# Performance work log

Measured on AMD Instinct MI355X. Metric: run time of the kernel, lower is better.

The kernel has to match this reference:

```python
import jax, jax.numpy as jnp
import numpy as np

N_NODES = 100000
F_DIM = 128
D_LAT = 64
N_EDGES = 1000000
H_DIM = 128


def setup_inputs() -> dict:
    key = jax.random.key(0)
    ks = jax.random.split(key, 10)
    rng = np.random.default_rng(0)
    # positive edges (random graph) and non-edge negative pairs (dedup vs edge set,
    # mirroring the membership check in the torch elbo loop)
    edges = rng.integers(0, N_NODES, size=(2, N_EDGES))
    edge_hash = edges[0].astype(np.int64) * N_NODES + edges[1]
    cand = rng.integers(0, N_NODES, size=(2, 2 * N_EDGES))
    cand_hash = cand[0].astype(np.int64) * N_NODES + cand[1]
    keep = ~np.isin(cand_hash, edge_hash)
    neg = cand[:, keep][:, :N_EDGES]
    r = lambda k, s, sc=1.0: jax.random.normal(k, s, jnp.float32) * sc
    return {
        "x": r(ks[0], (N_NODES, F_DIM)),
        "eps": r(ks[1], (N_NODES, D_LAT)),
        "W_mu": r(ks[2], (F_DIM, D_LAT), 0.05),
        "b_mu": jnp.zeros((D_LAT,), jnp.float32),
        "W_lv": r(ks[3], (F_DIM, D_LAT), 0.05),
        "b_lv": jnp.zeros((D_LAT,), jnp.float32),
        "W1": r(ks[4], (D_LAT, H_DIM), 0.1),
        "b1": jnp.zeros((H_DIM,), jnp.float32),
        "W2": r(ks[5], (H_DIM, 1), 0.1),
        "b2": jnp.zeros((1,), jnp.float32),
        "edge_index": jnp.asarray(edges, jnp.int64) if jax.config.jax_enable_x64 else jnp.asarray(edges, jnp.int32),
        "neg_index": jnp.asarray(neg, jnp.int64) if jax.config.jax_enable_x64 else jnp.asarray(neg, jnp.int32),
    }


def reference(x, eps, W_mu, b_mu, W_lv, b_lv, W1, b1, W2, b2, edge_index, neg_index):
    # encoder: per-node diagonal Gaussian q(z|x)
    mu = x @ W_mu + b_mu            # [N, D]
    logvar = x @ W_lv + b_lv        # [N, D]
    z = mu + eps * jnp.exp(0.5 * logvar)  # q.rsample()

    def pair_logits(idx):
        zu = z[idx[0]]              # [E, D] gather
        zv = z[idx[1]]
        h = jax.nn.relu((zu * zv) @ W1 + b1)  # [E, H]
        return (h @ W2 + b2)[:, 0]  # [E]

    # Bernoulli(logits).log_prob(1) = log_sigmoid(l); log(1 - sigmoid(l)) = log_sigmoid(-l)
    true_lp = jax.nn.log_sigmoid(pair_logits(edge_index))
    false_lp = jax.nn.log_sigmoid(-pair_logits(neg_index))
    recon = jnp.mean(jnp.concatenate([true_lp, false_lp]))

    # KL(q || N(0, I)) per node, mean over nodes
    kl = jnp.mean(0.5 * jnp.sum(jnp.square(mu) + jnp.exp(logvar) - 1.0 - logvar, axis=-1))
    return -(recon - kl)
```

## Files before the change

kernel.cpp:

```cpp
#include <hip/hip_runtime.h>
#include <math.h>

#define F_DIM 128
#define D_LAT 64
#define H_DIM 128

typedef __attribute__((ext_vector_type(8))) short bf16x8;
typedef __attribute__((ext_vector_type(4))) float f32x4;
typedef __attribute__((ext_vector_type(2))) float f32x2;

__device__ __forceinline__ unsigned short f2bf(float f) {
    unsigned int u = __builtin_bit_cast(unsigned int, f);
    return (unsigned short)((u + 0x8000u) >> 16);
}

__device__ __forceinline__ long prod_fp8(unsigned long long qu, unsigned long long qv) {
    const unsigned int ul = (unsigned int)qu, uh = (unsigned int)(qu >> 32);
    const unsigned int vl = (unsigned int)qv, vh = (unsigned int)(qv >> 32);
    const f32x2 u01 = __builtin_amdgcn_cvt_pk_f32_fp8(ul, false);
    const f32x2 u23 = __builtin_amdgcn_cvt_pk_f32_fp8(ul, true);
    const f32x2 u45 = __builtin_amdgcn_cvt_pk_f32_fp8(uh, false);
    const f32x2 u67 = __builtin_amdgcn_cvt_pk_f32_fp8(uh, true);
    const f32x2 v01 = __builtin_amdgcn_cvt_pk_f32_fp8(vl, false);
    const f32x2 v23 = __builtin_amdgcn_cvt_pk_f32_fp8(vl, true);
    const f32x2 v45 = __builtin_amdgcn_cvt_pk_f32_fp8(vh, false);
    const f32x2 v67 = __builtin_amdgcn_cvt_pk_f32_fp8(vh, true);
    const f32x2 p01 = u01 * v01, p23 = u23 * v23;
    const f32x2 p45 = u45 * v45, p67 = u67 * v67;
    unsigned int r0 = __builtin_amdgcn_cvt_pk_fp8_f32(p01[0], p01[1], 0u, false);
    r0 = __builtin_amdgcn_cvt_pk_fp8_f32(p23[0], p23[1], r0, true);
    unsigned int r1 = __builtin_amdgcn_cvt_pk_fp8_f32(p45[0], p45[1], 0u, false);
    r1 = __builtin_amdgcn_cvt_pk_fp8_f32(p67[0], p67[1], r1, true);
    return (long)(((unsigned long long)r1 << 32) | r0);
}

__global__ __launch_bounds__(256) void enc_mfma_kernel(
    const float* __restrict__ x, const float* __restrict__ eps,
    const float* __restrict__ Wmu, const float* __restrict__ bmu,
    const float* __restrict__ Wlv, const float* __restrict__ blv,
    unsigned char* __restrict__ zb, float* __restrict__ accum, int nNodes)
{
    const int lane = threadIdx.x & 63;
    const int li   = lane & 15;
    const int gi   = lane >> 4;

    bf16x8 wf[8][4];
#pragma unroll
    for (int t = 0; t < 4; ++t)
#pragma unroll
        for (int s = 0; s < 4; ++s)
#pragma unroll
            for (int j = 0; j < 8; ++j) {
                const int k = s * 32 + gi * 8 + j;
                wf[t][s][j]     = (short)f2bf(Wmu[k * D_LAT + 16 * t + li]);
                wf[t + 4][s][j] = (short)f2bf(Wlv[k * D_LAT + 16 * t + li]);
            }
    float bmu4[4], blv4[4];
#pragma unroll
    for (int t = 0; t < 4; ++t) {
        bmu4[t] = bmu[16 * t + li];
        blv4[t] = blv[16 * t + li];
    }

    const int wid = (blockIdx.x * blockDim.x + threadIdx.x) >> 6;
    const int nw  = (gridDim.x * blockDim.x) >> 6;
    const int NB  = nNodes >> 4;

    float klacc = 0.f;
    for (int nb = wid; nb < NB; nb += nw) {
        const int nbase = nb << 4;
        const float* __restrict__ xrow = x + (size_t)(nbase + li) * F_DIM;

        bf16x8 af[4];
#pragma unroll
        for (int s = 0; s < 4; ++s) {
            const f32x4 v0 = *(const f32x4*)(xrow + s * 32 + gi * 8);
            const f32x4 v1 = *(const f32x4*)(xrow + s * 32 + gi * 8 + 4);
#pragma unroll
            for (int j = 0; j < 4; ++j) {
                af[s][j]     = (short)f2bf(v0[j]);
                af[s][j + 4] = (short)f2bf(v1[j]);
            }
        }

        f32x4 acc[8];
#pragma unroll
        for (int t = 0; t < 4; ++t) {
            acc[t]     = (f32x4){bmu4[t], bmu4[t], bmu4[t], bmu4[t]};
            acc[t + 4] = (f32x4){blv4[t], blv4[t], blv4[t], blv4[t]};
        }
#pragma unroll
        for (int t = 0; t < 8; ++t)
#pragma unroll
            for (int s = 0; s < 4; ++s)
                acc[t] = __builtin_amdgcn_mfma_f32_16x16x32_bf16(af[s], wf[t][s], acc[t], 0, 0, 0);

#pragma unroll
        for (int r = 0; r < 4; ++r) {
            const int row = nbase + gi * 4 + r;
#pragma unroll
            for (int t = 0; t < 4; ++t) {
                const float mu  = acc[t][r];
                const float lv  = acc[t + 4][r];
                const float e05 = __expf(0.5f * lv);
                klacc += mu * mu + e05 * e05 - 1.0f - lv;
                const float zv = fmaf(eps[(size_t)row * D_LAT + 16 * t + li], e05, mu);
                zb[(size_t)row * D_LAT + 16 * t + li] =
                    (unsigned char)(__builtin_amdgcn_cvt_pk_fp8_f32(zv, 0.f, 0u, false) & 0xffu);
            }
        }
    }
    for (int off = 32; off; off >>= 1) klacc += __shfl_xor(klacc, off);
    if (lane == 0) atomicAdd(&accum[1], 0.5f * klacc);
}

__global__ __launch_bounds__(256) void edge_mfma_kernel(
    const unsigned char* __restrict__ zb,
    const int* __restrict__ eidx, const int* __restrict__ nidx,
    const float* __restrict__ W1, const float* __restrict__ b1,
    const float* __restrict__ W2, const float* __restrict__ b2,
    float* __restrict__ accum, int E)
{
    const int lane = threadIdx.x & 63;
    const int li   = lane & 15;
    const int gi   = lane >> 4;

    long w1q[8][2];
#pragma unroll
    for (int t = 0; t < 8; ++t)
#pragma unroll
        for (int s = 0; s < 2; ++s) {
            float f[8];
#pragma unroll
            for (int j = 0; j < 8; ++j)
                f[j] = W1[(32 * s + gi * 8 + j) * H_DIM + 16 * t + li];
            unsigned int r0 = __builtin_amdgcn_cvt_pk_fp8_f32(f[0], f[1], 0u, false);
            r0 = __builtin_amdgcn_cvt_pk_fp8_f32(f[2], f[3], r0, true);
            unsigned int r1 = __builtin_amdgcn_cvt_pk_fp8_f32(f[4], f[5], 0u, false);
            r1 = __builtin_amdgcn_cvt_pk_fp8_f32(f[6], f[7], r1, true);
            w1q[t][s] = (long)(((unsigned long long)r1 << 32) | r0);
        }
    float b1r[8], w2r[8];
#pragma unroll
    for (int t = 0; t < 8; ++t) {
        b1r[t] = b1[16 * t + li];
        w2r[t] = W2[16 * t + li];
    }
    const float b2v = b2[0];

    const int wid = (blockIdx.x * blockDim.x + threadIdx.x) >> 6;
    const int nw  = (gridDim.x * blockDim.x) >> 6;
    const int NBpos = E >> 4;
    const int NB    = NBpos << 1;
    const int NBH   = NB >> 1;

    float lp = 0.f;

    int cu0, cv0, cu1, cv1;
    {
        const int hb  = (wid < NBH) ? wid : (NBH - 1);
        const int pb0 = 2 * hb, pb1 = 2 * hb + 1;
        const int* __restrict__ i0 = (pb0 < NBpos) ? eidx : nidx;
        const int* __restrict__ i1 = (pb1 < NBpos) ? eidx : nidx;
        const int m0 = ((pb0 < NBpos) ? pb0 : pb0 - NBpos) << 4;
        const int m1 = ((pb1 < NBpos) ? pb1 : pb1 - NBpos) << 4;
        cu0 = i0[m0 + li]; cv0 = i0[E + m0 + li];
        cu1 = i1[m1 + li]; cv1 = i1[E + m1 + li];
    }

    for (int hb = wid; hb < NBH; hb += nw) {
        const int pb0 = 2 * hb, pb1 = 2 * hb + 1;

        const unsigned long long* zu0 = (const unsigned long long*)(zb + (size_t)cu0 * D_LAT + gi * 8);
        const unsigned long long* zv0 = (const unsigned long long*)(zb + (size_t)cv0 * D_LAT + gi * 8);
        const unsigned long long* zu1 = (const unsigned long long*)(zb + (size_t)cu1 * D_LAT + gi * 8);
        const unsigned long long* zv1 = (const unsigned long long*)(zb + (size_t)cv1 * D_LAT + gi * 8);
        const unsigned long long qu00 = zu0[0], qu01 = zu0[4];
        const unsigned long long qv00 = zv0[0], qv01 = zv0[4];
        const unsigned long long qu10 = zu1[0], qu11 = zu1[4];
        const unsigned long long qv10 = zv1[0], qv11 = zv1[4];

        int nu0, nv0, nu1, nv1;
        {
            const int hn  = (hb + nw < NBH) ? hb + nw : hb;
            const int qb0 = 2 * hn, qb1 = 2 * hn + 1;
            const int* __restrict__ i0 = (qb0 < NBpos) ? eidx : nidx;
            const int* __restrict__ i1 = (qb1 < NBpos) ? eidx : nidx;
            const int m0 = ((qb0 < NBpos) ? qb0 : qb0 - NBpos) << 4;
            const int m1 = ((qb1 < NBpos) ? qb1 : qb1 - NBpos) << 4;
            nu0 = i0[m0 + li]; nv0 = i0[E + m0 + li];
            nu1 = i1[m1 + li]; nv1 = i1[E + m1 + li];
        }

#pragma unroll
        for (int blk = 0; blk < 2; ++blk) {
            const long pa0 = prod_fp8(blk ? qu10 : qu00, blk ? qv10 : qv00);
            const long pa1 = prod_fp8(blk ? qu11 : qu01, blk ? qv11 : qv01);
            f32x4 acc[8];
#pragma unroll
            for (int t = 0; t < 8; ++t)
                acc[t] = (f32x4){b1r[t], b1r[t], b1r[t], b1r[t]};
#pragma unroll
            for (int t = 0; t < 8; ++t) {
                acc[t] = __builtin_amdgcn_mfma_f32_16x16x32_fp8_fp8(pa0, w1q[t][0], acc[t], 0, 0, 0);
                acc[t] = __builtin_amdgcn_mfma_f32_16x16x32_fp8_fp8(pa1, w1q[t][1], acc[t], 0, 0, 0);
            }
            float t0 = 0.f, t1 = 0.f, t2 = 0.f, t3 = 0.f;
#pragma unroll
            for (int t = 0; t < 8; ++t) {
                t0 += fmaxf(acc[t][0], 0.f) * w2r[t];
                t1 += fmaxf(acc[t][1], 0.f) * w2r[t];
                t2 += fmaxf(acc[t][2], 0.f) * w2r[t];
                t3 += fmaxf(acc[t][3], 0.f) * w2r[t];
            }
#pragma unroll
            for (int off = 1; off < 16; off <<= 1) {
                t0 += __shfl_xor(t0, off);
                t1 += __shfl_xor(t1, off);
                t2 += __shfl_xor(t2, off);
                t3 += __shfl_xor(t3, off);
            }
            const int pb = blk ? pb1 : pb0;
            const float sg = (pb < NBpos) ? 1.f : -1.f;
            const float l0 = sg * (t0 + b2v), l1 = sg * (t1 + b2v);
            const float l2 = sg * (t2 + b2v), l3 = sg * (t3 + b2v);
            lp += fminf(l0, 0.f) - __logf(1.f + __expf(-fabsf(l0)));
            lp += fminf(l1, 0.f) - __logf(1.f + __expf(-fabsf(l1)));
            lp += fminf(l2, 0.f) - __logf(1.f + __expf(-fabsf(l2)));
            lp += fminf(l3, 0.f) - __logf(1.f + __expf(-fabsf(l3)));
        }

        cu0 = nu0; cv0 = nv0; cu1 = nu1; cv1 = nv1;
    }
    for (int off = 32; off; off >>= 1) lp += __shfl_xor(lp, off);
    if (lane == 0) atomicAdd(&accum[0], lp * 0.0625f);
}

__global__ void fin_kernel(const float* __restrict__ accum, float* __restrict__ out,
                           int nNodes, int E)
{
    const float recon = accum[0] / (float)(2 * E);
    const float kl    = accum[1] / (float)nNodes;
    out[0] = kl - recon;
}

extern "C" void kernel_launch(void* const* d_in, const int* in_sizes, int n_in,
                              void* d_out, int out_size, void* d_ws, size_t ws_size,
                              hipStream_t stream)
{
    const float* x    = (const float*)d_in[0];
    const float* eps  = (const float*)d_in[1];
    const float* Wmu  = (const float*)d_in[2];
    const float* bmu  = (const float*)d_in[3];
    const float* Wlv  = (const float*)d_in[4];
    const float* blv  = (const float*)d_in[5];
    const float* W1   = (const float*)d_in[6];
    const float* b1   = (const float*)d_in[7];
    const float* W2   = (const float*)d_in[8];
    const float* b2   = (const float*)d_in[9];
    const int*   eidx = (const int*)d_in[10];
    const int*   nidx = (const int*)d_in[11];

    const int nNodes = in_sizes[1] / D_LAT;
    const int E      = in_sizes[10] / 2;

    float* accum      = (float*)d_ws;
    unsigned char* zb = (unsigned char*)((char*)d_ws + 256);

    hipMemsetAsync(d_ws, 0, 256, stream);
    enc_mfma_kernel<<<512, 256, 0, stream>>>(x, eps, Wmu, bmu, Wlv, blv, zb, accum, nNodes);
    edge_mfma_kernel<<<2048, 256, 0, stream>>>(zb, eidx, nidx, W1, b1, W2, b2, accum, E);
    fin_kernel<<<1, 1, 0, stream>>>(accum, (float*)d_out, nNodes, E);
}
```

Before: 213.6 us.

## Prefetch gathered z rows one iteration ahead and use 16-byte row loads

The edge loop now issues the z-row gathers for the next pair of 16-edge blocks before computing the current blocks. Index loads are prefetched two iterations ahead, so gather latency overlaps with the MFMA and reduction work. Each lane fetches a contiguous 16-byte slice of the row instead of two 8-byte pieces, and the W1 fragment layout is permuted to match the new K ordering. This costs extra registers for the in-flight row buffers, which may reduce occupancy.

```diff
diff --git a/kernel.cpp b/kernel.cpp
--- a/kernel.cpp
+++ b/kernel.cpp
@@ -8,6 +8,7 @@
 typedef __attribute__((ext_vector_type(8))) short bf16x8;
 typedef __attribute__((ext_vector_type(4))) float f32x4;
 typedef __attribute__((ext_vector_type(2))) float f32x2;
+typedef __attribute__((ext_vector_type(2))) unsigned long long u64x2;
 
 __device__ __forceinline__ unsigned short f2bf(float f) {
     unsigned int u = __builtin_bit_cast(unsigned int, f);
@@ -133,7 +134,7 @@
             float f[8];
 #pragma unroll
             for (int j = 0; j < 8; ++j)
-                f[j] = W1[(32 * s + gi * 8 + j) * H_DIM + 16 * t + li];
+                f[j] = W1[(gi * 16 + s * 8 + j) * H_DIM + 16 * t + li];
             unsigned int r0 = __builtin_amdgcn_cvt_pk_fp8_f32(f[0], f[1], 0u, false);
             r0 = __builtin_amdgcn_cvt_pk_fp8_f32(f[2], f[3], r0, true);
             unsigned int r1 = __builtin_amdgcn_cvt_pk_fp8_f32(f[4], f[5], 0u, false);
@@ -151,87 +152,77 @@
     const int wid = (blockIdx.x * blockDim.x + threadIdx.x) >> 6;
     const int nw  = (gridDim.x * blockDim.x) >> 6;
     const int NBpos = E >> 4;
-    const int NB    = NBpos << 1;
-    const int NBH   = NB >> 1;
+    const int NBH   = NBpos;
 
     float lp = 0.f;
 
-    int cu0, cv0, cu1, cv1;
-    {
-        const int hb  = (wid < NBH) ? wid : (NBH - 1);
-        const int pb0 = 2 * hb, pb1 = 2 * hb + 1;
+    auto load_idx = [&](int hb, int& u0, int& v0, int& u1, int& v1) {
+        const int h   = (hb < NBH) ? hb : (NBH - 1);
+        const int pb0 = 2 * h, pb1 = 2 * h + 1;
         const int* __restrict__ i0 = (pb0 < NBpos) ? eidx : nidx;
         const int* __restrict__ i1 = (pb1 < NBpos) ? eidx : nidx;
         const int m0 = ((pb0 < NBpos) ? pb0 : pb0 - NBpos) << 4;
         const int m1 = ((pb1 < NBpos) ? pb1 : pb1 - NBpos) << 4;
-        cu0 = i0[m0 + li]; cv0 = i0[E + m0 + li];
-        cu1 = i1[m1 + li]; cv1 = i1[E + m1 + li];
-    }
-
+        u0 = i0[m0 + li]; v0 = i0[E + m0 + li];
+        u1 = i1[m1 + li]; v1 = i1[E + m1 + li];
+    };
+    auto load_row = [&](int node) -> u64x2 {
+        return *(const u64x2*)(zb + (size_t)node * D_LAT + (gi << 4));
+    };
+    auto do_block = [&](u64x2 qu, u64x2 qv, bool pos) {
+        const long pa0 = prod_fp8(qu[0], qv[0]);
+        const long pa1 = prod_fp8(qu[1], qv[1]);
+        f32x4 acc[8];
+#pragma unroll
+        for (int t = 0; t < 8; ++t)
+            acc[t] = (f32x4){b1r[t], b1r[t], b1r[t], b1r[t]};
+#pragma unroll
+        for (int t = 0; t < 8; ++t) {
+            acc[t] = __builtin_amdgcn_mfma_f32_16x16x32_fp8_fp8(pa0, w1q[t][0], acc[t], 0, 0, 0);
+            acc[t] = __builtin_amdgcn_mfma_f32_16x16x32_fp8_fp8(pa1, w1q[t][1], acc[t], 0, 0, 0);
+        }
+        float t0 = 0.f, t1 = 0.f, t2 = 0.f, t3 = 0.f;
+#pragma unroll
+        for (int t = 0; t < 8; ++t) {
+            t0 += fmaxf(acc[t][0], 0.f) * w2r[t];
+            t1 += fmaxf(acc[t][1], 0.f) * w2r[t];
+            t2 += fmaxf(acc[t][2], 0.f) * w2r[t];
+            t3 += fmaxf(acc[t][3], 0.f) * w2r[t];
+        }
+#pragma unroll
+        for (int off = 1; off < 16; off <<= 1) {
+            t0 += __shfl_xor(t0, off);
+            t1 += __shfl_xor(t1, off);
+            t2 += __shfl_xor(t2, off);
+            t3 += __shfl_xor(t3, off);
+        }
+        const float sg = pos ? 1.f : -1.f;
+        const float l0 = sg * (t0 + b2v), l1 = sg * (t1 + b2v);
+        const float l2 = sg * (t2 + b2v), l3 = sg * (t3 + b2v);
+        lp += fminf(l0, 0.f) - __logf(1.f + __expf(-fabsf(l0)));
+        lp += fminf(l1, 0.f) - __logf(1.f + __expf(-fabsf(l1)));
+        lp += fminf(l2, 0.f) - __logf(1.f + __expf(-fabsf(l2)));
+        lp += fminf(l3, 0.f) - __logf(1.f + __expf(-fabsf(l3)));
+    };
+
+    int ju0, jv0, ju1, jv1;
+    load_idx(wid, ju0, jv0, ju1, jv1);
+    u64x2 A0u = load_row(ju0), A0v = load_row(jv0);
+    u64x2 A1u = load_row(ju1), A1v = load_row(jv1);
+    load_idx(wid + nw, ju0, jv0, ju1, jv1);
+
+#pragma unroll 2
     for (int hb = wid; hb < NBH; hb += nw) {
-        const int pb0 = 2 * hb, pb1 = 2 * hb + 1;
-
-        const unsigned long long* zu0 = (const unsigned long long*)(zb + (size_t)cu0 * D_LAT + gi * 8);
-        const unsigned long long* zv0 = (const unsigned long long*)(zb + (size_t)cv0 * D_LAT + gi * 8);
-        const unsigned long long* zu1 = (const unsigned long long*)(zb + (size_t)cu1 * D_LAT + gi * 8);
-        const unsigned long long* zv1 = (const unsigned long long*)(zb + (size_t)cv1 * D_LAT + gi * 8);
-        const unsigned long long qu00 = zu0[0], qu01 = zu0[4];
-        const unsigned long long qv00 = zv0[0], qv01 = zv0[4];
-        const unsigned long long qu10 = zu1[0], qu11 = zu1[4];
-        const unsigned long long qv10 = zv1[0], qv11 = zv1[4];
-
-        int nu0, nv0, nu1, nv1;
-        {
-            const int hn  = (hb + nw < NBH) ? hb + nw : hb;
-            const int qb0 = 2 * hn, qb1 = 2 * hn + 1;
-            const int* __restrict__ i0 = (qb0 < NBpos) ? eidx : nidx;
-            const int* __restrict__ i1 = (qb1 < NBpos) ? eidx : nidx;
-            const int m0 = ((qb0 < NBpos) ? qb0 : qb0 - NBpos) << 4;
-            const int m1 = ((qb1 < NBpos) ? qb1 : qb1 - NBpos) << 4;
-            nu0 = i0[m0 + li]; nv0 = i0[E + m0 + li];
-            nu1 = i1[m1 + li]; nv1 = i1[E + m1 + li];
-        }
-
-#pragma unroll
-        for (int blk = 0; blk < 2; ++blk) {
-            const long pa0 = prod_fp8(blk ? qu10 : qu00, blk ? qv10 : qv00);
-            const long pa1 = prod_fp8(blk ? qu11 : qu01, blk ? qv11 : qv01);
-            f32x4 acc[8];
-#pragma unroll
-            for (int t = 0; t < 8; ++t)
-                acc[t] = (f32x4){b1r[t], b1r[t], b1r[t], b1r[t]};
-#pragma unroll
-            for (int t = 0; t < 8; ++t) {
-                acc[t] = __builtin_amdgcn_mfma_f32_16x16x32_fp8_fp8(pa0, w1q[t][0], acc[t], 0, 0, 0);
-                acc[t] = __builtin_amdgcn_mfma_f32_16x16x32_fp8_fp8(pa1, w1q[t][1], acc[t], 0, 0, 0);
-            }
-            float t0 = 0.f, t1 = 0.f, t2 = 0.f, t3 = 0.f;
-#pragma unroll
-            for (int t = 0; t < 8; ++t) {
-                t0 += fmaxf(acc[t][0], 0.f) * w2r[t];
-                t1 += fmaxf(acc[t][1], 0.f) * w2r[t];
-                t2 += fmaxf(acc[t][2], 0.f) * w2r[t];
-                t3 += fmaxf(acc[t][3], 0.f) * w2r[t];
-            }
-#pragma unroll
-            for (int off = 1; off < 16; off <<= 1) {
-                t0 += __shfl_xor(t0, off);
-                t1 += __shfl_xor(t1, off);
-                t2 += __shfl_xor(t2, off);
-                t3 += __shfl_xor(t3, off);
-            }
-            const int pb = blk ? pb1 : pb0;
-            const float sg = (pb < NBpos) ? 1.f : -1.f;
-            const float l0 = sg * (t0 + b2v), l1 = sg * (t1 + b2v);
-            const float l2 = sg * (t2 + b2v), l3 = sg * (t3 + b2v);
-            lp += fminf(l0, 0.f) - __logf(1.f + __expf(-fabsf(l0)));
-            lp += fminf(l1, 0.f) - __logf(1.f + __expf(-fabsf(l1)));
-            lp += fminf(l2, 0.f) - __logf(1.f + __expf(-fabsf(l2)));
-            lp += fminf(l3, 0.f) - __logf(1.f + __expf(-fabsf(l3)));
-        }
-
-        cu0 = nu0; cv0 = nv0; cu1 = nu1; cv1 = nv1;
-    }
+        u64x2 B0u = load_row(ju0), B0v = load_row(jv0);
+        u64x2 B1u = load_row(ju1), B1v = load_row(jv1);
+        int ku0, kv0, ku1, kv1;
+        load_idx(hb + 2 * nw, ku0, kv0, ku1, kv1);
+        do_block(A0u, A0v, 2 * hb < NBpos);
+        do_block(A1u, A1v, 2 * hb + 1 < NBpos);
+        A0u = B0u; A0v = B0v; A1u = B1u; A1v = B1v;
+        ju0 = ku0; jv0 = kv0; ju1 = ku1; jv1 = kv1;
+    }
+
     for (int off = 32; off; off >>= 1) lp += __shfl_xor(lp, off);
     if (lane == 0) atomicAdd(&accum[0], lp * 0.0625f);
 }
```

After: 202.4 us. -5.2%, faster.
